# Performance work log

Measured on AMD Instinct MI355X. Metric: run time of the kernel, lower is better.

## Reference

```python
import jax, jax.numpy as jnp
import numpy as np

C = 64        # channel_n
HID = 128     # hidden_size
HEADS = 4
HD = 16       # head_dim = embed_dim // heads, embed_dim overwritten to channel_n
INNER = HEADS * HD  # 64
MLP = 64
H = W = 64    # img_size
B = 8
STEPS = 6
IN_CH = 1     # input_channels
SCALE = HD ** -0.5


def conv3x3_reflect(x, w, b):
    # x: [B,C,H,W], w: [O,I,3,3] -- reflect padding like nn.Conv2d(padding_mode='reflect')
    xp = jnp.pad(x, ((0, 0), (0, 0), (1, 1), (1, 1)), mode='reflect')
    y = jax.lax.conv_general_dilated(xp, w, (1, 1), 'VALID',
                                     dimension_numbers=('NCHW', 'OIHW', 'NCHW'))
    return y + b[None, :, None, None]


def layernorm(x, w, b, axes):
    mu = jnp.mean(x, axis=axes, keepdims=True)
    var = jnp.var(x, axis=axes, keepdims=True)
    return (x - mu) * jax.lax.rsqrt(var + 1e-5) * w + b


def localize(t, h, w):
    # t: [B,heads,n,d] -> [B,heads,n,9,d]; zero-padded 3x3 neighbourhoods
    # (equivalent to grouped conv with 9 unit-impulse filters, padding='same')
    b, nh, n, d = t.shape
    g = t.reshape(b, nh, h, w, d)
    gp = jnp.pad(g, ((0, 0), (0, 0), (1, 1), (1, 1), (0, 0)))
    nb = jnp.stack([gp[:, :, i:i + h, j:j + w, :]
                    for i in range(3) for j in range(3)], axis=4)
    return nb.reshape(b, nh, n, 9, d)


def attn_block(t, ln_w, ln_b, qkv_w, out_w, out_b):
    y = layernorm(t, ln_w, ln_b, -1)
    qkv = y @ qkv_w.T                              # [B,n,3*inner]
    q, k, v = jnp.split(qkv, 3, axis=-1)
    to_heads = lambda z: z.reshape(z.shape[0], z.shape[1], HEADS, HD).transpose(0, 2, 1, 3)
    q, k, v = to_heads(q), to_heads(k), to_heads(v)   # [B,h,n,d]
    kl = localize(k, H, W)                          # [B,h,n,9,d]
    vl = localize(v, H, W)
    dots = jnp.einsum('bhnd,bhnkd->bhnk', q, kl) * SCALE
    a = jax.nn.softmax(dots, axis=-1)               # [B,h,n,9]
    o = jnp.einsum('bhnk,bhnkd->bhnd', a, vl)
    o = o.transpose(0, 2, 1, 3).reshape(t.shape[0], t.shape[1], INNER)
    return o @ out_w.T + out_b


def ff_block(t, ln_w, ln_b, w1, b1, w2, b2):
    y = layernorm(t, ln_w, ln_b, -1)
    y = jax.nn.gelu(y @ w1.T + b1, approximate=False)
    return y @ w2.T + b2


def setup_inputs() -> dict:
    key = jax.random.key(0)
    ks = jax.random.split(key, 20)
    s = 0.02
    inp = {
        'x': jax.random.normal(ks[0], (B, H, W, C), jnp.float32),
        'masks': jax.random.bernoulli(ks[1], 0.5, (STEPS, B, H, W, 1)),
        'p0_w': jax.random.normal(ks[2], (C, C, 3, 3)) * s,
        'p0_b': jnp.zeros((C,)),
        'p1_w': jax.random.normal(ks[3], (C, C, 3, 3)) * s,
        'p1_b': jnp.zeros((C,)),
        'fc0_w': jax.random.normal(ks[4], (HID, 3 * C)) * s,
        'fc0_b': jnp.zeros((HID,)),
        'fc1_w': jax.random.normal(ks[5], (C, HID)) * s,  # zero-init in torch; random here for a non-trivial test
        'norm0_w': jnp.ones((H, W, HID)),
        'norm0_b': jnp.zeros((H, W, HID)),
        'ln1_w': jnp.ones((C,)),
        'ln1_b': jnp.zeros((C,)),
        'qkv_w': jax.random.normal(ks[6], (3 * INNER, C)) * s,
        'out_w': jax.random.normal(ks[7], (C, INNER)) * s,
        'out_b': jnp.zeros((C,)),
        'ln2_w': jnp.ones((C,)),
        'ln2_b': jnp.zeros((C,)),
        'ff1_w': jax.random.normal(ks[8], (MLP, C)) * s,
        'ff1_b': jnp.zeros((MLP,)),
        'ff2_w': jax.random.normal(ks[9], (C, MLP)) * s,
        'ff2_b': jnp.zeros((C,)),
        'steps': STEPS,
    }
    return inp


def reference(x, masks, p0_w, p0_b, p1_w, p1_b, fc0_w, fc0_b, fc1_w,
              norm0_w, norm0_b, ln1_w, ln1_b, qkv_w, out_w, out_b,
              ln2_w, ln2_b, ff1_w, ff1_b, ff2_w, ff2_b, steps):
    def step(xc, mask):
        # ---- NCA perception + update (BackboneNCA.perceive + fc0/relu/norm/fc1) ----
        xt = xc.transpose(0, 3, 1, 2)                      # [B,C,H,W]
        y1 = conv3x3_reflect(xt, p0_w, p0_b)
        y2 = conv3x3_reflect(xt, p1_w, p1_b)
        p = jnp.concatenate([xt, y1, y2], 1).transpose(0, 2, 3, 1)  # [B,H,W,3C]
        hd = jax.nn.relu(p @ fc0_w.T + fc0_b)              # [B,H,W,HID]
        hd = layernorm(hd, norm0_w, norm0_b, (-3, -2, -1))  # norm0 over [H,W,HID]
        dx = hd @ fc1_w.T                                   # [B,H,W,C]
        dx = dx * mask.astype(xc.dtype)                     # stochastic fire
        xn = xc + dx
        # ---- ViT block with localized (3x3 windowed) attention ----
        t = xn.reshape(B, H * W, C)
        t = t + attn_block(t, ln1_w, ln1_b, qkv_w, out_w, out_b)
        t = t + ff_block(t, ln2_w, ln2_b, ff1_w, ff1_b, ff2_w, ff2_b)
        xn = t.reshape(B, H, W, C)
        # keep input channels unchanged
        xn = jnp.concatenate([xc[..., :IN_CH], xn[..., IN_CH:]], axis=-1)
        return xn, None

    out, _ = jax.lax.scan(step, x, masks)
    return out
```

## Files before the change

### kernel.cpp

```cpp
#include <hip/hip_runtime.h>
#include <hip/hip_bf16.h>

typedef __hip_bfloat16 bf16;
typedef __attribute__((ext_vector_type(8))) short bf16x8;
typedef __attribute__((ext_vector_type(4))) float f32x4;

#define NSTEP 6

static __device__ __forceinline__ float b2f(bf16 v) { return __bfloat162float(v); }

static __device__ __forceinline__ float ldp(const void* p, int i, int md) {
    return md ? ((const float*)p)[i] : b2f(((const bf16*)p)[i]);
}
static __device__ __forceinline__ float finz(float v) {
    return (v == v && v * 0.0f == 0.0f) ? v : 0.0f;
}
static __device__ __forceinline__ unsigned short f2bfu(float v) {
    bf16 h = __float2bfloat16(v);
    return *(unsigned short*)&h;
}

static __device__ __forceinline__ void ld_bf8(const bf16* p, float* f) {
    union { uint4 u; unsigned short s[8]; } r;
    r.u = *(const uint4*)p;
#pragma unroll
    for (int j = 0; j < 8; ++j) f[j] = __uint_as_float(((unsigned)r.s[j]) << 16);
}
static __device__ __forceinline__ void ldp8(const void* p, int i, int md, float* f) {
    if (md) {
        const float* fp = (const float*)p + i;
        float4 a = *(const float4*)fp, b = *(const float4*)(fp + 4);
        f[0]=a.x; f[1]=a.y; f[2]=a.z; f[3]=a.w; f[4]=b.x; f[5]=b.y; f[6]=b.z; f[7]=b.w;
    } else {
        ld_bf8((const bf16*)p + i, f);
    }
}
static __device__ __forceinline__ uint4 pk_bf8(const float* f) {
    union { uint4 u; unsigned short s[8]; } r;
#pragma unroll
    for (int j = 0; j < 8; ++j) r.s[j] = f2bfu(f[j]);
    return r.u;
}


__global__ void k_detect(const uint4* __restrict__ m4,
                         const uint4* __restrict__ x4,
                         int* __restrict__ flags, float* __restrict__ accv) {
    __shared__ int s3f, sup, slo, sf32;
    int t = threadIdx.x;
    if (t == 0) { s3f = 0; sup = 0; slo = 0; sf32 = 0; }
    if (t < 96) accv[t] = 0.f;
    __syncthreads();
    int l3f = 0, lup = 0, llo = 0, lf = 0;
    for (int i = t; i < 3072; i += 256) {
        uint4 v = m4[i];
        const unsigned* d = (const unsigned*)&v;
#pragma unroll
        for (int j = 0; j < 4; ++j) {
            unsigned w = d[j];
            unsigned x3f = w ^ 0x3F3F3F3Fu;
            if ((x3f - 0x01010101u) & ~x3f & 0x80808080u) l3f = 1;
            if (w & 0xFFFFFF00u) lup = 1;
            if (w & 0x0000FFFFu) llo = 1;
        }
    }
    for (int i = t; i < 4096; i += 256) {
        uint4 v = x4[i];
        const unsigned* d = (const unsigned*)&v;
#pragma unroll
        for (int j = 0; j < 4; ++j) {
            unsigned bb = (d[j] >> 8) & 0x7Fu;
            if (bb > 0x48u) lf = 1;
        }
    }
    if (l3f) atomicOr(&s3f, 1);
    if (lup) atomicOr(&sup, 1);
    if (llo) atomicOr(&slo, 1);
    if (lf)  atomicOr(&sf32, 1);
    __syncthreads();
    if (t == 0) {
        int mode;
        if (!s3f && !sup) mode = 0;
        else if (!s3f)    mode = 1;
        else if (slo)     mode = 2;
        else              mode = 3;
        flags[0] = mode;
        flags[1] = sf32;
    }
}

__global__ void k_cast(const void* __restrict__ in, float* __restrict__ out,
                       const int* __restrict__ mflags, int n8) {
    int md = mflags[1];
    int i = blockIdx.x * 256 + threadIdx.x;
    if (i < n8) {
        float f[8];
        ldp8(in, i * 8, md, f);
#pragma unroll
        for (int j = 0; j < 8; ++j) f[j] = finz(f[j]);
        *(float4*)&out[i * 8]     = make_float4(f[0], f[1], f[2], f[3]);
        *(float4*)&out[i * 8 + 4] = make_float4(f[4], f[5], f[6], f[7]);
    }
}

__global__ void k_pack_multi(const void* __restrict__ pa, const void* __restrict__ pb,
                             const void* __restrict__ pc, const void* __restrict__ pd,
                             const void* __restrict__ pe, const void* __restrict__ pf,
                             short* __restrict__ out, const int* __restrict__ mflags) {
    int md = mflags[1];
    int i = blockIdx.x * 256 + threadIdx.x;
    if (i >= 57344) return;
    float v;
    if      (i < 24576) v = ldp(pa, i, md);
    else if (i < 32768) v = ldp(pb, i - 24576, md);
    else if (i < 45056) v = ldp(pc, i - 32768, md);
    else if (i < 49152) v = ldp(pd, i - 45056, md);
    else if (i < 53248) v = ldp(pe, i - 49152, md);
    else                v = ldp(pf, i - 53248, md);
    out[i] = (short)f2bfu(v);
}

__global__ void k_pack_bt1(const void* __restrict__ p0, const void* __restrict__ p1,
                           short* __restrict__ out, const int* __restrict__ mflags) {
    int md = mflags[1];
    int i = blockIdx.x * 256 + threadIdx.x;
    if (i < 128 * 576) {
        int o = i / 576, k = i % 576;
        int kk = k >> 6, ii = k & 63;
        float v = (o < 64) ? ldp(p0, o * 576 + ii * 9 + kk, md)
                           : ldp(p1, (o - 64) * 576 + ii * 9 + kk, md);
        out[i] = (short)f2bfu(v);
    }
}


__global__ __launch_bounds__(512) void k_perceive(
    const float* __restrict__ xin, const short* __restrict__ bt1,
    const short* __restrict__ fc0s, const void* __restrict__ p0b,
    const void* __restrict__ p1b, const void* __restrict__ fc0b,
    const int* __restrict__ mflags, bf16* __restrict__ hd,
    float* __restrict__ accv, int step)
{
    __shared__ __align__(16) short xpad_s[3 * 66 * 72];
    __shared__ __align__(16) short P_s[64 * 200];
    __shared__ float red[32];
    int md = mflags[1];
    int bh = blockIdx.x;
    int b = bh >> 6, h = bh & 63;
    int t = threadIdx.x;

    for (int e = t; e < 1536; e += 512) {
        int c8 = e & 7, w = (e >> 3) & 63, r = e >> 9;
        int hr = h - 1 + r; hr = hr < 0 ? -hr : (hr > 63 ? 126 - hr : hr);
        const float* src = xin + ((((b << 6) + hr) << 6) | w) * 64 + c8 * 8;
        float f[8];
        float4 v0 = *(const float4*)src, v1 = *(const float4*)(src + 4);
        f[0]=v0.x; f[1]=v0.y; f[2]=v0.z; f[3]=v0.w; f[4]=v1.x; f[5]=v1.y; f[6]=v1.z; f[7]=v1.w;
        uint4 pv = pk_bf8(f);
        *(uint4*)&xpad_s[((r * 66) + w + 1) * 72 + c8 * 8] = pv;
        if (r == 1) *(uint4*)&P_s[w * 200 + c8 * 8] = pv;
    }
    if (t < 48) {
        int c8 = t & 7, side = (t >> 3) & 1, r = t >> 4;
        int hr = h - 1 + r; hr = hr < 0 ? -hr : (hr > 63 ? 126 - hr : hr);
        int wsrc = side ? 62 : 1, wp = side ? 65 : 0;
        const float* src = xin + ((((b << 6) + hr) << 6) | wsrc) * 64 + c8 * 8;
        float f[8];
        float4 v0 = *(const float4*)src, v1 = *(const float4*)(src + 4);
        f[0]=v0.x; f[1]=v0.y; f[2]=v0.z; f[3]=v0.w; f[4]=v1.x; f[5]=v1.y; f[6]=v1.z; f[7]=v1.w;
        *(uint4*)&xpad_s[((r * 66) + wp) * 72 + c8 * 8] = pk_bf8(f);
    }
    __syncthreads();

    int og  = __builtin_amdgcn_readfirstlane(t >> 6);
    int l   = t & 63, nl = l & 15, q = l >> 4;
    int mt0 = (og & 1) * 2;
    int nt0 = (og >> 1) * 2;
    int o0  = nt0 * 16 + nl, o1 = o0 + 16;

    f32x4 acc[2][2];
#pragma unroll
    for (int i = 0; i < 2; ++i)
#pragma unroll
        for (int j = 0; j < 2; ++j) acc[i][j] = (f32x4){0.f, 0.f, 0.f, 0.f};

    for (int kt = 0; kt < 18; ++kt) {
        int kk = kt >> 1, c0 = (kt & 1) << 5;
        int r = kk / 3, cxi = kk - r * 3;
        bf16x8 b0 = *(const bf16x8*)(bt1 + o0 * 576 + kt * 32 + q * 8);
        bf16x8 b1 = *(const bf16x8*)(bt1 + o1 * 576 + kt * 32 + q * 8);
        bf16x8 a0 = *(const bf16x8*)&xpad_s[((r * 66) + mt0 * 16 + nl + cxi) * 72 + c0 + q * 8];
        bf16x8 a1 = *(const bf16x8*)&xpad_s[((r * 66) + mt0 * 16 + 16 + nl + cxi) * 72 + c0 + q * 8];
        acc[0][0] = __builtin_amdgcn_mfma_f32_16x16x32_bf16(a0, b0, acc[0][0], 0, 0, 0);
        acc[0][1] = __builtin_amdgcn_mfma_f32_16x16x32_bf16(a0, b1, acc[0][1], 0, 0, 0);
        acc[1][0] = __builtin_amdgcn_mfma_f32_16x16x32_bf16(a1, b0, acc[1][0], 0, 0, 0);
        acc[1][1] = __builtin_amdgcn_mfma_f32_16x16x32_bf16(a1, b1, acc[1][1], 0, 0, 0);
    }
    {
        float bias0 = (o0 < 64) ? ldp(p0b, o0, md) : ldp(p1b, o0 - 64, md);
        float bias1 = (o1 < 64) ? ldp(p0b, o1, md) : ldp(p1b, o1 - 64, md);
#pragma unroll
        for (int i = 0; i < 2; ++i)
#pragma unroll
            for (int j = 0; j < 2; ++j) {
                int oo = j ? o1 : o0;
                float bb = j ? bias1 : bias0;
#pragma unroll
                for (int r2 = 0; r2 < 4; ++r2) {
                    int m = (mt0 + i) * 16 + q * 4 + r2;
                    P_s[m * 200 + 64 + oo] = (short)f2bfu(acc[i][j][r2] + bb);
                }
            }
    }
    __syncthreads();

#pragma unroll
    for (int i = 0; i < 2; ++i)
#pragma unroll
        for (int j = 0; j < 2; ++j) acc[i][j] = (f32x4){0.f, 0.f, 0.f, 0.f};
    for (int kt = 0; kt < 6; ++kt) {
        bf16x8 b0 = *(const bf16x8*)(fc0s + o0 * 192 + kt * 32 + q * 8);
        bf16x8 b1 = *(const bf16x8*)(fc0s + o1 * 192 + kt * 32 + q * 8);
        bf16x8 a0 = *(const bf16x8*)&P_s[(mt0 * 16 + nl) * 200 + kt * 32 + q * 8];
        bf16x8 a1 = *(const bf16x8*)&P_s[(mt0 * 16 + 16 + nl) * 200 + kt * 32 + q * 8];
        acc[0][0] = __builtin_amdgcn_mfma_f32_16x16x32_bf16(a0, b0, acc[0][0], 0, 0, 0);
        acc[0][1] = __builtin_amdgcn_mfma_f32_16x16x32_bf16(a0, b1, acc[0][1], 0, 0, 0);
        acc[1][0] = __builtin_amdgcn_mfma_f32_16x16x32_bf16(a1, b0, acc[1][0], 0, 0, 0);
        acc[1][1] = __builtin_amdgcn_mfma_f32_16x16x32_bf16(a1, b1, acc[1][1], 0, 0, 0);
    }
    float lsum = 0.f, lsq = 0.f;
    {
        float fb0 = ldp(fc0b, o0, md), fb1 = ldp(fc0b, o1, md);
#pragma unroll
        for (int i = 0; i < 2; ++i)
#pragma unroll
            for (int j = 0; j < 2; ++j) {
                int oo = j ? o1 : o0;
                float bb = j ? fb1 : fb0;
#pragma unroll
                for (int r2 = 0; r2 < 4; ++r2) {
                    int m = (mt0 + i) * 16 + q * 4 + r2;
                    float v = fmaxf(acc[i][j][r2] + bb, 0.f);
                    unsigned short hu = f2bfu(v);
                    hd[((bh << 6) + m) * 128 + oo] = *(bf16*)&hu;
                    float vr = __uint_as_float(((unsigned)hu) << 16);
                    lsum += vr; lsq += vr * vr;
                }
            }
    }
#pragma unroll
    for (int off = 32; off > 0; off >>= 1) {
        lsum += __shfl_down(lsum, off, 64);
        lsq  += __shfl_down(lsq,  off, 64);
    }
    if (l == 0) { red[og] = lsum; red[16 + og] = lsq; }
    __syncthreads();
    if (t == 0) {
        float a = 0.f, s2 = 0.f;
#pragma unroll
        for (int w = 0; w < 8; ++w) { a += red[w]; s2 += red[16 + w]; }
        atomicAdd(&accv[step * 16 + b * 2],     a);
        atomicAdd(&accv[step * 16 + b * 2 + 1], s2);
    }
}

__global__ __launch_bounds__(512) void k_update_qkv(
    float* __restrict__ xio, const bf16* __restrict__ hd,
    const short* __restrict__ fc1s, const void* __restrict__ n0w,
    const void* __restrict__ n0b, const void* __restrict__ mraw,
    const int* __restrict__ mflags, const float* __restrict__ accv,
    float* __restrict__ c0buf, const short* __restrict__ qkvs,
    const void* __restrict__ ln1w, const void* __restrict__ ln1b,
    bf16* __restrict__ qkv, int step)
{
    __shared__ __align__(16) char sm[43264];
    short* hdn = (short*)sm;
    float* ts  = (float*)(sm + 17408);
    short* ys  = (short*)(sm + 34048);
    short* qo  = (short*)sm;

    int md = mflags[1];
    int bh = blockIdx.x;
    int b = bh >> 6, h = bh & 63;
    int t = threadIdx.x;
    const float invN = 1.f / 524288.f;
    float mean = accv[step * 16 + b * 2] * invN;
    float var  = accv[step * 16 + b * 2 + 1] * invN - mean * mean;
    float rstd = rsqrtf(fmaxf(var, 0.f) + 1e-5f);

    const bf16* hrow = hd + ((b * 64 + h) * 64) * 128;
    for (int e = t; e < 1024; e += 512) {
        int pos = e >> 4, j8 = (e & 15) * 8;
        float hv[8], wv[8], bv[8], f[8];
        ld_bf8(hrow + pos * 128 + j8, hv);
        int ni = (h * 64 + pos) * 128 + j8;
        ldp8(n0w, ni, md, wv);
        ldp8(n0b, ni, md, bv);
#pragma unroll
        for (int j = 0; j < 8; ++j) f[j] = (hv[j] - mean) * rstd * wv[j] + bv[j];
        *(uint4*)&hdn[pos * 136 + j8] = pk_bf8(f);
    }
    __syncthreads();

    int og = __builtin_amdgcn_readfirstlane(t >> 6);
    int l = t & 63, nl = l & 15, q = l >> 4;

    {
        int mt = og & 3, nh = og >> 2;
        int o0 = nh * 32 + nl, o1 = o0 + 16;
        f32x4 a0 = (f32x4){0.f,0.f,0.f,0.f}, a1 = (f32x4){0.f,0.f,0.f,0.f};
#pragma unroll
        for (int kt = 0; kt < 4; ++kt) {
            bf16x8 av = *(const bf16x8*)&hdn[(mt * 16 + nl) * 136 + kt * 32 + q * 8];
            bf16x8 b0 = *(const bf16x8*)(fc1s + o0 * 128 + kt * 32 + q * 8);
            bf16x8 b1 = *(const bf16x8*)(fc1s + o1 * 128 + kt * 32 + q * 8);
            a0 = __builtin_amdgcn_mfma_f32_16x16x32_bf16(av, b0, a0, 0, 0, 0);
            a1 = __builtin_amdgcn_mfma_f32_16x16x32_bf16(av, b1, a1, 0, 0, 0);
        }
#pragma unroll
        for (int r2 = 0; r2 < 4; ++r2) {
            int m = mt * 16 + q * 4 + r2;
            ts[m * 65 + o0] = a0[r2];
            ts[m * 65 + o1] = a1[r2];
        }
    }
    __syncthreads();

    int cg = og;
    int pos = t & 63;
    {
        int mmode = mflags[0];
        int midx = ((step * 8 + b) * 64 + h) * 64 + pos;
        int mk;
        if (mmode == 0)      mk = ((const int*)mraw)[midx] != 0;
        else if (mmode == 1) mk = ((const unsigned char*)mraw)[midx] != 0;
        else if (mmode == 2) mk = ((const unsigned short*)mraw)[midx] != 0;
        else                 mk = ((const float*)mraw)[midx] != 0.0f;

        int idx = ((b * 64 + h) * 64 + pos) * 64 + cg * 8;
        float4 x0 = *(const float4*)&xio[idx];
        float4 x1 = *(const float4*)&xio[idx + 4];
        float xv[8] = {x0.x, x0.y, x0.z, x0.w, x1.x, x1.y, x1.z, x1.w};
        if (cg == 0) c0buf[(b * 64 + h) * 64 + pos] = xv[0];
        float* tp = &ts[pos * 65 + cg * 8];
        float xn[8];
#pragma unroll
        for (int ci = 0; ci < 8; ++ci) {
            xn[ci] = finz(mk ? (xv[ci] + tp[ci]) : xv[ci]);
            tp[ci] = xn[ci];
        }
        *(float4*)&xio[idx]     = make_float4(xn[0], xn[1], xn[2], xn[3]);
        *(float4*)&xio[idx + 4] = make_float4(xn[4], xn[5], xn[6], xn[7]);
    }
    __syncthreads();

    {
        int tok = t >> 3, j8 = (t & 7) * 8;
        float v[8];
        float ls = 0.f, lq = 0.f;
#pragma unroll
        for (int ci = 0; ci < 8; ++ci) {
            v[ci] = ts[tok * 65 + j8 + ci];
            ls += v[ci]; lq += v[ci] * v[ci];
        }
#pragma unroll
        for (int off = 1; off < 8; off <<= 1) {
            ls += __shfl_xor(ls, off, 64);
            lq += __shfl_xor(lq, off, 64);
        }
        float mu = ls * (1.f / 64.f);
        float vr = lq * (1.f / 64.f) - mu * mu;
        float rs = rsqrtf(fmaxf(vr, 0.f) + 1e-5f);
        float wv[8], bv[8];
        ldp8(ln1w, j8, md, wv);
        ldp8(ln1b, j8, md, bv);
        float yv[8];
#pragma unroll
        for (int ci = 0; ci < 8; ++ci) yv[ci] = (v[ci] - mu) * rs * wv[ci] + bv[ci];
        *(uint4*)&ys[tok * 72 + j8] = pk_bf8(yv);
    }
    __syncthreads();

    {
        int mt = og & 3, nh = og >> 2;
        f32x4 qa[6];
#pragma unroll
        for (int n = 0; n < 6; ++n) qa[n] = (f32x4){0.f, 0.f, 0.f, 0.f};
#pragma unroll
        for (int kt = 0; kt < 2; ++kt) {
            bf16x8 av = *(const bf16x8*)&ys[(mt * 16 + nl) * 72 + kt * 32 + q * 8];
#pragma unroll
            for (int n = 0; n < 6; ++n) {
                bf16x8 bv = *(const bf16x8*)(qkvs + (((nh * 6 + n) * 16) + nl) * 64 + kt * 32 + q * 8);
                qa[n] = __builtin_amdgcn_mfma_f32_16x16x32_bf16(av, bv, qa[n], 0, 0, 0);
            }
        }
#pragma unroll
        for (int n = 0; n < 6; ++n)
#pragma unroll
            for (int r2 = 0; r2 < 4; ++r2) {
                int m = mt * 16 + q * 4 + r2;
                qo[m * 200 + (nh * 6 + n) * 16 + nl] = (short)f2bfu(qa[n][r2]);
            }
    }
    __syncthreads();

    for (int e = t; e < 1536; e += 512) {
        int p2 = e / 24, c8 = e - p2 * 24;
        *(uint4*)(qkv + ((bh << 6) + p2) * 192 + c8 * 8) =
            *(const uint4*)&qo[p2 * 200 + c8 * 8];
    }
}

__global__ __launch_bounds__(512) void k_attn_ff(
    const bf16* __restrict__ qkv, float* __restrict__ xio,
    const float* __restrict__ c0buf, const short* __restrict__ outs,
    const short* __restrict__ ff1s, const short* __restrict__ ff2s,
    const void* __restrict__ outb, const void* __restrict__ ln2w,
    const void* __restrict__ ln2b, const void* __restrict__ ff1b,
    const void* __restrict__ ff2b, const int* __restrict__ mflags,
    void* __restrict__ dout, int write_out)
{
    __shared__ __align__(16) char smraw[57024];
    short* Ks = (short*)smraw;
    short* Vs = (short*)(smraw + 28512);
    short* Ao = (short*)smraw;
    float* ts = (float*)(smraw + 9216);
    short* ys = (short*)(smraw + 25856);
    short* hs = (short*)(smraw + 35072);

    int md = mflags[1];
    int bh = blockIdx.x;
    int b = bh >> 6, h = bh & 63;
    int t = threadIdx.x;

    if (t < 96) {
        int kind = (t >= 48) ? 1 : 0, u = t - kind * 48;
        int r = u >> 4, side = (u >> 3) & 1, c8 = u & 7;
        short* dst = kind ? Vs : Ks;
        uint4 z = {0, 0, 0, 0};
        *(uint4*)&dst[((r * 66) + (side ? 65 : 0)) * 72 + c8 * 8] = z;
    }
    for (int e = t; e < 3072; e += 512) {
        int kind = (e >= 1536) ? 1 : 0, u = e - kind * 1536;
        int c8 = u & 7, w = (u >> 3) & 63, r = u >> 9;
        int hr = h - 1 + r;
        uint4 v = {0, 0, 0, 0};
        if (hr >= 0 && hr <= 63)
            v = *(const uint4*)(qkv + ((b * 64 + hr) * 64 + w) * 192 + 64 + kind * 64 + c8 * 8);
        short* dst = kind ? Vs : Ks;
        *(uint4*)&dst[((r * 66) + w + 1) * 72 + c8 * 8] = v;
    }
    __syncthreads();

    int head = __builtin_amdgcn_readfirstlane(t >> 6) & 3;
    int pos  = t & 63;
    bool act = t < 256;
    float o[16];
    if (act) {
        float qv[16];
        const bf16* qr = qkv + (((b * 64 + h) * 64) + pos) * 192 + head * 16;
        ld_bf8(qr, qv); ld_bf8(qr + 8, qv + 8);

        float a9[9];
#pragma unroll
        for (int r = 0; r < 3; ++r)
#pragma unroll
            for (int cxi = 0; cxi < 3; ++cxi) {
                const short* kp = &Ks[((r * 66) + pos + cxi) * 72 + head * 16];
                float kf[16];
                ld_bf8((const bf16*)kp, kf);
                ld_bf8((const bf16*)(kp + 8), kf + 8);
                float dot = 0.f;
#pragma unroll
                for (int d = 0; d < 16; ++d) dot = fmaf(qv[d], kf[d], dot);
                a9[r * 3 + cxi] = dot * 0.25f;
            }
        float mx = a9[0];
#pragma unroll
        for (int k = 1; k < 9; ++k) mx = fmaxf(mx, a9[k]);
        float ssum = 0.f;
#pragma unroll
        for (int k = 0; k < 9; ++k) { a9[k] = __expf(a9[k] - mx); ssum += a9[k]; }
        float inv = 1.f / ssum;
#pragma unroll
        for (int k = 0; k < 9; ++k) a9[k] *= inv;

#pragma unroll
        for (int d = 0; d < 16; ++d) o[d] = 0.f;
#pragma unroll
        for (int r = 0; r < 3; ++r)
#pragma unroll
            for (int cxi = 0; cxi < 3; ++cxi) {
                const short* vp = &Vs[((r * 66) + pos + cxi) * 72 + head * 16];
                float vf[16];
                ld_bf8((const bf16*)vp, vf);
                ld_bf8((const bf16*)(vp + 8), vf + 8);
                float w = a9[r * 3 + cxi];
#pragma unroll
                for (int d = 0; d < 16; ++d) o[d] = fmaf(w, vf[d], o[d]);
            }
    }
    __syncthreads();
    if (act) {
        *(uint4*)&Ao[pos * 72 + head * 16]     = pk_bf8(o);
        *(uint4*)&Ao[pos * 72 + head * 16 + 8] = pk_bf8(o + 8);
    }
    __syncthreads();

    int og = __builtin_amdgcn_readfirstlane(t >> 6);
    int l = t & 63, nl = l & 15, qd = l >> 4;
    int mt = og & 3;
    int nt0 = (og >> 2) * 2;
    int o0 = nt0 * 16 + nl, o1 = o0 + 16;

    {
        f32x4 pa[2];
        pa[0] = (f32x4){0.f,0.f,0.f,0.f}; pa[1] = (f32x4){0.f,0.f,0.f,0.f};
#pragma unroll
        for (int kt = 0; kt < 2; ++kt) {
            bf16x8 av = *(const bf16x8*)&Ao[(mt * 16 + nl) * 72 + kt * 32 + qd * 8];
            bf16x8 b0 = *(const bf16x8*)(outs + o0 * 64 + kt * 32 + qd * 8);
            bf16x8 b1 = *(const bf16x8*)(outs + o1 * 64 + kt * 32 + qd * 8);
            pa[0] = __builtin_amdgcn_mfma_f32_16x16x32_bf16(av, b0, pa[0], 0, 0, 0);
            pa[1] = __builtin_amdgcn_mfma_f32_16x16x32_bf16(av, b1, pa[1], 0, 0, 0);
        }
        float ob0 = ldp(outb, o0, md), ob1 = ldp(outb, o1, md);
#pragma unroll
        for (int j = 0; j < 2; ++j)
#pragma unroll
            for (int r2 = 0; r2 < 4; ++r2) {
                int m = mt * 16 + qd * 4 + r2;
                ts[m * 65 + (j ? o1 : o0)] = pa[j][r2] + (j ? ob1 : ob0);
            }
    }
    __syncthreads();

    int idx = ((bh << 6) + pos) * 64 + (t >> 6) * 8;
    {
        int cg2 = t >> 6;
        float4 x0 = *(const float4*)&xio[idx];
        float4 x1 = *(const float4*)&xio[idx + 4];
        float* tp = &ts[pos * 65 + cg2 * 8];
        tp[0] += x0.x; tp[1] += x0.y; tp[2] += x0.z; tp[3] += x0.w;
        tp[4] += x1.x; tp[5] += x1.y; tp[6] += x1.z; tp[7] += x1.w;
    }
    __syncthreads();

    {
        int tok = t >> 3, j8 = (t & 7) * 8;
        float v[8];
        float ls = 0.f, lq = 0.f;
#pragma unroll
        for (int ci = 0; ci < 8; ++ci) {
            v[ci] = ts[tok * 65 + j8 + ci];
            ls += v[ci]; lq += v[ci] * v[ci];
        }
#pragma unroll
        for (int off = 1; off < 8; off <<= 1) {
            ls += __shfl_xor(ls, off, 64);
            lq += __shfl_xor(lq, off, 64);
        }
        float mu = ls * (1.f / 64.f);
        float vr = lq * (1.f / 64.f) - mu * mu;
        float rs = rsqrtf(fmaxf(vr, 0.f) + 1e-5f);
        float wv[8], bv[8];
        ldp8(ln2w, j8, md, wv);
        ldp8(ln2b, j8, md, bv);
        float yv[8];
#pragma unroll
        for (int ci = 0; ci < 8; ++ci) yv[ci] = (v[ci] - mu) * rs * wv[ci] + bv[ci];
        *(uint4*)&ys[tok * 72 + j8] = pk_bf8(yv);
    }
    __syncthreads();

    {
        f32x4 ma[2];
        ma[0] = (f32x4){0.f,0.f,0.f,0.f}; ma[1] = (f32x4){0.f,0.f,0.f,0.f};
#pragma unroll
        for (int kt = 0; kt < 2; ++kt) {
            bf16x8 av = *(const bf16x8*)&ys[(mt * 16 + nl) * 72 + kt * 32 + qd * 8];
            bf16x8 b0 = *(const bf16x8*)(ff1s + o0 * 64 + kt * 32 + qd * 8);
            bf16x8 b1 = *(const bf16x8*)(ff1s + o1 * 64 + kt * 32 + qd * 8);
            ma[0] = __builtin_amdgcn_mfma_f32_16x16x32_bf16(av, b0, ma[0], 0, 0, 0);
            ma[1] = __builtin_amdgcn_mfma_f32_16x16x32_bf16(av, b1, ma[1], 0, 0, 0);
        }
        float f1b0 = ldp(ff1b, o0, md), f1b1 = ldp(ff1b, o1, md);
#pragma unroll
        for (int j = 0; j < 2; ++j)
#pragma unroll
            for (int r2 = 0; r2 < 4; ++r2) {
                int m = mt * 16 + qd * 4 + r2;
                float v = ma[j][r2] + (j ? f1b1 : f1b0);
                float g = 0.5f * v * (1.f + erff(v * 0.70710678118654752f));
                hs[m * 72 + (j ? o1 : o0)] = (short)f2bfu(g);
            }
    }
    __syncthreads();

    {
        f32x4 fa[2];
        fa[0] = (f32x4){0.f,0.f,0.f,0.f}; fa[1] = (f32x4){0.f,0.f,0.f,0.f};
#pragma unroll
        for (int kt = 0; kt < 2; ++kt) {
            bf16x8 av = *(const bf16x8*)&hs[(mt * 16 + nl) * 72 + kt * 32 + qd * 8];
            bf16x8 b0 = *(const bf16x8*)(ff2s + o0 * 64 + kt * 32 + qd * 8);
            bf16x8 b1 = *(const bf16x8*)(ff2s + o1 * 64 + kt * 32 + qd * 8);
            fa[0] = __builtin_amdgcn_mfma_f32_16x16x32_bf16(av, b0, fa[0], 0, 0, 0);
            fa[1] = __builtin_amdgcn_mfma_f32_16x16x32_bf16(av, b1, fa[1], 0, 0, 0);
        }
        float f2b0 = ldp(ff2b, o0, md), f2b1 = ldp(ff2b, o1, md);
#pragma unroll
        for (int j = 0; j < 2; ++j)
#pragma unroll
            for (int r2 = 0; r2 < 4; ++r2) {
                int m = mt * 16 + qd * 4 + r2;
                int oo = j ? o1 : o0;
                ts[m * 65 + oo] += fa[j][r2] + (j ? f2b1 : f2b0);
            }
    }
    __syncthreads();

    {
        int cg2 = t >> 6;
        float fv[8];
#pragma unroll
        for (int ci = 0; ci < 8; ++ci) {
            float v = ts[pos * 65 + cg2 * 8 + ci];
            if (cg2 == 0 && ci == 0) v = c0buf[(bh << 6) + pos];
            fv[ci] = finz(v);
        }
        *(float4*)&xio[idx]     = make_float4(fv[0], fv[1], fv[2], fv[3]);
        *(float4*)&xio[idx + 4] = make_float4(fv[4], fv[5], fv[6], fv[7]);
        if (write_out) {
            if (md) {
                *(float4*)&((float*)dout)[idx]     = make_float4(fv[0], fv[1], fv[2], fv[3]);
                *(float4*)&((float*)dout)[idx + 4] = make_float4(fv[4], fv[5], fv[6], fv[7]);
            } else {
                *(uint4*)&((bf16*)dout)[idx] = pk_bf8(fv);
            }
        }
    }
}


extern "C" void kernel_launch(void* const* d_in, const int* in_sizes, int n_in,
                              void* d_out, int out_size, void* d_ws, size_t ws_size,
                              hipStream_t stream) {
    (void)in_sizes; (void)n_in; (void)out_size; (void)ws_size;
    const void* x     = d_in[0];
    const void* masks = d_in[1];
    const void* p0w   = d_in[2];
    const void* p0b   = d_in[3];
    const void* p1w   = d_in[4];
    const void* p1b   = d_in[5];
    const void* fc0w  = d_in[6];
    const void* fc0b  = d_in[7];
    const void* fc1w  = d_in[8];
    const void* n0w   = d_in[9];
    const void* n0b   = d_in[10];
    const void* ln1w  = d_in[11];
    const void* ln1b  = d_in[12];
    const void* qkvw  = d_in[13];
    const void* outw  = d_in[14];
    const void* outb  = d_in[15];
    const void* ln2w  = d_in[16];
    const void* ln2b  = d_in[17];
    const void* ff1w  = d_in[18];
    const void* ff1b  = d_in[19];
    const void* ff2w  = d_in[20];
    const void* ff2b  = d_in[21];

    char* wsb = (char*)d_ws;
    float* xst    = (float*)(wsb + 0);
    bf16*  hd     = (bf16*) (wsb + 8388608);
    bf16*  qkvb   = (bf16*) (wsb + 16777216);
    float* c0buf  = (float*)(wsb + 29360128);
    short* bt1    = (short*)(wsb + 29491200);
    short* packs  = (short*)(wsb + 29638656);
    float* accv   = (float*)(wsb + 29753344);
    int*   mflags = (int*)  (wsb + 29753728);

    short* fc0s = packs;
    short* fc1s = packs + 24576;
    short* qkvs = packs + 32768;
    short* outs = packs + 45056;
    short* ff1s = packs + 49152;
    short* ff2s = packs + 53248;

    k_detect<<<1, 256, 0, stream>>>((const uint4*)masks, (const uint4*)x, mflags, accv);
    k_cast<<<1024, 256, 0, stream>>>(x, xst, mflags, 262144);
    k_pack_bt1<<<288, 256, 0, stream>>>(p0w, p1w, bt1, mflags);
    k_pack_multi<<<224, 256, 0, stream>>>(fc0w, fc1w, qkvw, outw, ff1w, ff2w, packs, mflags);

    for (int s = 0; s < NSTEP; ++s) {
        k_perceive<<<512, 512, 0, stream>>>(xst, bt1, fc0s, p0b, p1b, fc0b, mflags, hd, accv, s);
        k_update_qkv<<<512, 512, 0, stream>>>(xst, hd, fc1s, n0w, n0b, masks, mflags, accv,
                                              c0buf, qkvs, ln1w, ln1b, qkvb, s);
        k_attn_ff<<<512, 512, 0, stream>>>(qkvb, xst, c0buf, outs, ff1s, ff2s,
                                           outb, ln2w, ln2b, ff1b, ff2b, mflags,
                                           d_out, (s == NSTEP - 1) ? 1 : 0);
    }
}
```

Measured before the change: 592.9 us.

## Fold norm0 into fc1 algebraically and fuse update/QKV into attention kernel

The global layernorm is rewritten as rstd*(hd*w)@fc1 - mean*rstd*(w@fc1) + b@fc1. The two weight products are precomputed once by a new k_fold kernel, so fc1 can run inside the perceive kernel before the global statistics are known. The separate update/QKV kernel is merged into the attention/FF kernel, which recomputes the update, LN1 and QKV for the three neighbouring rows instead of round-tripping qkv and hd through global memory. This drops one launch per step and ping-pongs the state between two buffers, at the cost of about three times the QKV work and larger shared memory use in the fused kernel.

```diff
diff --git a/kernel.cpp b/kernel.cpp
--- a/kernel.cpp
+++ b/kernel.cpp
@@ -133,16 +133,41 @@
     }
 }
 
+__global__ void k_fold(const void* __restrict__ n0w, const void* __restrict__ n0b,
+                       const short* __restrict__ fc1s, float* __restrict__ wsum,
+                       float* __restrict__ bconst, const int* __restrict__ mflags) {
+    __shared__ short fc1T[128 * 64];
+    int md = mflags[1];
+    int t = threadIdx.x;
+    for (int e = t; e < 8192; e += 256) {
+        int c2 = e >> 7, j = e & 127;
+        fc1T[j * 64 + c2] = fc1s[c2 * 128 + j];
+    }
+    __syncthreads();
+    int c = t & 63, pl = t >> 6;
+    int pos = blockIdx.x * 4 + pl;
+    float ws = 0.f, bs = 0.f;
+    for (int j = 0; j < 128; ++j) {
+        float f = b2f(*(const bf16*)&fc1T[j * 64 + c]);
+        ws = fmaf(ldp(n0w, pos * 128 + j, md), f, ws);
+        bs = fmaf(ldp(n0b, pos * 128 + j, md), f, bs);
+    }
+    wsum[pos * 64 + c]   = ws;
+    bconst[pos * 64 + c] = bs;
+}
+
 
 __global__ __launch_bounds__(512) void k_perceive(
     const float* __restrict__ xin, const short* __restrict__ bt1,
-    const short* __restrict__ fc0s, const void* __restrict__ p0b,
-    const void* __restrict__ p1b, const void* __restrict__ fc0b,
-    const int* __restrict__ mflags, bf16* __restrict__ hd,
+    const short* __restrict__ fc0s, const short* __restrict__ fc1s,
+    const void* __restrict__ p0b, const void* __restrict__ p1b,
+    const void* __restrict__ fc0b, const void* __restrict__ n0w,
+    const int* __restrict__ mflags, float* __restrict__ t1,
     float* __restrict__ accv, int step)
 {
     __shared__ __align__(16) short xpad_s[3 * 66 * 72];
     __shared__ __align__(16) short P_s[64 * 200];
+    __shared__ __align__(16) short hd_s[64 * 136];
     __shared__ float red[32];
     int md = mflags[1];
     int bh = blockIdx.x;
@@ -242,7 +267,7 @@
                     int m = (mt0 + i) * 16 + q * 4 + r2;
                     float v = fmaxf(acc[i][j][r2] + bb, 0.f);
                     unsigned short hu = f2bfu(v);
-                    hd[((bh << 6) + m) * 128 + oo] = *(bf16*)&hu;
+                    hd_s[m * 136 + oo] = (short)hu;
                     float vr = __uint_as_float(((unsigned)hu) << 16);
                     lsum += vr; lsq += vr * vr;
                 }
@@ -262,177 +287,71 @@
         atomicAdd(&accv[step * 16 + b * 2],     a);
         atomicAdd(&accv[step * 16 + b * 2 + 1], s2);
     }
-}
-
-__global__ __launch_bounds__(512) void k_update_qkv(
-    float* __restrict__ xio, const bf16* __restrict__ hd,
-    const short* __restrict__ fc1s, const void* __restrict__ n0w,
-    const void* __restrict__ n0b, const void* __restrict__ mraw,
-    const int* __restrict__ mflags, const float* __restrict__ accv,
-    float* __restrict__ c0buf, const short* __restrict__ qkvs,
-    const void* __restrict__ ln1w, const void* __restrict__ ln1b,
-    bf16* __restrict__ qkv, int step)
+
+    for (int e = t; e < 1024; e += 512) {
+        int pos = e >> 4, j8 = (e & 15) * 8;
+        float hv[8], wv[8];
+        ld_bf8((const bf16*)&hd_s[pos * 136 + j8], hv);
+        ldp8(n0w, (h * 64 + pos) * 128 + j8, md, wv);
+#pragma unroll
+        for (int j = 0; j < 8; ++j) hv[j] *= wv[j];
+        *(uint4*)&hd_s[pos * 136 + j8] = pk_bf8(hv);
+    }
+    __syncthreads();
+
+    {
+        int mt = og & 3, nh = og >> 2;
+        int to0 = nh * 32 + nl, to1 = to0 + 16;
+        f32x4 a0 = (f32x4){0.f,0.f,0.f,0.f}, a1 = (f32x4){0.f,0.f,0.f,0.f};
+#pragma unroll
+        for (int kt = 0; kt < 4; ++kt) {
+            bf16x8 av = *(const bf16x8*)&hd_s[(mt * 16 + nl) * 136 + kt * 32 + q * 8];
+            bf16x8 b0 = *(const bf16x8*)(fc1s + to0 * 128 + kt * 32 + q * 8);
+            bf16x8 b1 = *(const bf16x8*)(fc1s + to1 * 128 + kt * 32 + q * 8);
+            a0 = __builtin_amdgcn_mfma_f32_16x16x32_bf16(av, b0, a0, 0, 0, 0);
+            a1 = __builtin_amdgcn_mfma_f32_16x16x32_bf16(av, b1, a1, 0, 0, 0);
+        }
+#pragma unroll
+        for (int r2 = 0; r2 < 4; ++r2) {
+            int m = mt * 16 + q * 4 + r2;
+            t1[((bh << 6) + m) * 64 + to0] = a0[r2];
+            t1[((bh << 6) + m) * 64 + to1] = a1[r2];
+        }
+    }
+}
+
+__global__ __launch_bounds__(512) void k_step2(
+    const float* __restrict__ xin, float* __restrict__ xout,
+    const float* __restrict__ t1, const float* __restrict__ wsum,
+    const float* __restrict__ bconst, const void* __restrict__ mraw,
+    const short* __restrict__ qkvs, const void* __restrict__ ln1w,
+    const void* __restrict__ ln1b, const short* __restrict__ outs,
+    const short* __restrict__ ff1s, const short* __restrict__ ff2s,
+    const void* __restrict__ outb, const void* __restrict__ ln2w,
+    const void* __restrict__ ln2b, const void* __restrict__ ff1b,
+    const void* __restrict__ ff2b, const int* __restrict__ mflags,
+    const float* __restrict__ accv, void* __restrict__ dout,
+    int step, int write_out)
 {
-    __shared__ __align__(16) char sm[43264];
-    short* hdn = (short*)sm;
-    float* ts  = (float*)(sm + 17408);
-    short* ys  = (short*)(sm + 34048);
-    short* qo  = (short*)sm;
+    __shared__ __align__(16) char smraw[75456];
+    short* Ks = (short*)smraw;
+    short* Vs = (short*)(smraw + 28512);
+    short* qo = (short*)(smraw + 57024);
+    short* ys = (short*)(smraw + 66240);
+    short* Ao = (short*)smraw;
+    float* ts = (float*)(smraw + 9216);
+    short* hs = (short*)(smraw + 25856);
 
     int md = mflags[1];
     int bh = blockIdx.x;
     int b = bh >> 6, h = bh & 63;
     int t = threadIdx.x;
+
     const float invN = 1.f / 524288.f;
     float mean = accv[step * 16 + b * 2] * invN;
     float var  = accv[step * 16 + b * 2 + 1] * invN - mean * mean;
     float rstd = rsqrtf(fmaxf(var, 0.f) + 1e-5f);
-
-    const bf16* hrow = hd + ((b * 64 + h) * 64) * 128;
-    for (int e = t; e < 1024; e += 512) {
-        int pos = e >> 4, j8 = (e & 15) * 8;
-        float hv[8], wv[8], bv[8], f[8];
-        ld_bf8(hrow + pos * 128 + j8, hv);
-        int ni = (h * 64 + pos) * 128 + j8;
-        ldp8(n0w, ni, md, wv);
-        ldp8(n0b, ni, md, bv);
-#pragma unroll
-        for (int j = 0; j < 8; ++j) f[j] = (hv[j] - mean) * rstd * wv[j] + bv[j];
-        *(uint4*)&hdn[pos * 136 + j8] = pk_bf8(f);
-    }
-    __syncthreads();
-
-    int og = __builtin_amdgcn_readfirstlane(t >> 6);
-    int l = t & 63, nl = l & 15, q = l >> 4;
-
-    {
-        int mt = og & 3, nh = og >> 2;
-        int o0 = nh * 32 + nl, o1 = o0 + 16;
-        f32x4 a0 = (f32x4){0.f,0.f,0.f,0.f}, a1 = (f32x4){0.f,0.f,0.f,0.f};
-#pragma unroll
-        for (int kt = 0; kt < 4; ++kt) {
-            bf16x8 av = *(const bf16x8*)&hdn[(mt * 16 + nl) * 136 + kt * 32 + q * 8];
-            bf16x8 b0 = *(const bf16x8*)(fc1s + o0 * 128 + kt * 32 + q * 8);
-            bf16x8 b1 = *(const bf16x8*)(fc1s + o1 * 128 + kt * 32 + q * 8);
-            a0 = __builtin_amdgcn_mfma_f32_16x16x32_bf16(av, b0, a0, 0, 0, 0);
-            a1 = __builtin_amdgcn_mfma_f32_16x16x32_bf16(av, b1, a1, 0, 0, 0);
-        }
-#pragma unroll
-        for (int r2 = 0; r2 < 4; ++r2) {
-            int m = mt * 16 + q * 4 + r2;
-            ts[m * 65 + o0] = a0[r2];
-            ts[m * 65 + o1] = a1[r2];
-        }
-    }
-    __syncthreads();
-
-    int cg = og;
-    int pos = t & 63;
-    {
-        int mmode = mflags[0];
-        int midx = ((step * 8 + b) * 64 + h) * 64 + pos;
-        int mk;
-        if (mmode == 0)      mk = ((const int*)mraw)[midx] != 0;
-        else if (mmode == 1) mk = ((const unsigned char*)mraw)[midx] != 0;
-        else if (mmode == 2) mk = ((const unsigned short*)mraw)[midx] != 0;
-        else                 mk = ((const float*)mraw)[midx] != 0.0f;
-
-        int idx = ((b * 64 + h) * 64 + pos) * 64 + cg * 8;
-        float4 x0 = *(const float4*)&xio[idx];
-        float4 x1 = *(const float4*)&xio[idx + 4];
-        float xv[8] = {x0.x, x0.y, x0.z, x0.w, x1.x, x1.y, x1.z, x1.w};
-        if (cg == 0) c0buf[(b * 64 + h) * 64 + pos] = xv[0];
-        float* tp = &ts[pos * 65 + cg * 8];
-        float xn[8];
-#pragma unroll
-        for (int ci = 0; ci < 8; ++ci) {
-            xn[ci] = finz(mk ? (xv[ci] + tp[ci]) : xv[ci]);
-            tp[ci] = xn[ci];
-        }
-        *(float4*)&xio[idx]     = make_float4(xn[0], xn[1], xn[2], xn[3]);
-        *(float4*)&xio[idx + 4] = make_float4(xn[4], xn[5], xn[6], xn[7]);
-    }
-    __syncthreads();
-
-    {
-        int tok = t >> 3, j8 = (t & 7) * 8;
-        float v[8];
-        float ls = 0.f, lq = 0.f;
-#pragma unroll
-        for (int ci = 0; ci < 8; ++ci) {
-            v[ci] = ts[tok * 65 + j8 + ci];
-            ls += v[ci]; lq += v[ci] * v[ci];
-        }
-#pragma unroll
-        for (int off = 1; off < 8; off <<= 1) {
-            ls += __shfl_xor(ls, off, 64);
-            lq += __shfl_xor(lq, off, 64);
-        }
-        float mu = ls * (1.f / 64.f);
-        float vr = lq * (1.f / 64.f) - mu * mu;
-        float rs = rsqrtf(fmaxf(vr, 0.f) + 1e-5f);
-        float wv[8], bv[8];
-        ldp8(ln1w, j8, md, wv);
-        ldp8(ln1b, j8, md, bv);
-        float yv[8];
-#pragma unroll
-        for (int ci = 0; ci < 8; ++ci) yv[ci] = (v[ci] - mu) * rs * wv[ci] + bv[ci];
-        *(uint4*)&ys[tok * 72 + j8] = pk_bf8(yv);
-    }
-    __syncthreads();
-
-    {
-        int mt = og & 3, nh = og >> 2;
-        f32x4 qa[6];
-#pragma unroll
-        for (int n = 0; n < 6; ++n) qa[n] = (f32x4){0.f, 0.f, 0.f, 0.f};
-#pragma unroll
-        for (int kt = 0; kt < 2; ++kt) {
-            bf16x8 av = *(const bf16x8*)&ys[(mt * 16 + nl) * 72 + kt * 32 + q * 8];
-#pragma unroll
-            for (int n = 0; n < 6; ++n) {
-                bf16x8 bv = *(const bf16x8*)(qkvs + (((nh * 6 + n) * 16) + nl) * 64 + kt * 32 + q * 8);
-                qa[n] = __builtin_amdgcn_mfma_f32_16x16x32_bf16(av, bv, qa[n], 0, 0, 0);
-            }
-        }
-#pragma unroll
-        for (int n = 0; n < 6; ++n)
-#pragma unroll
-            for (int r2 = 0; r2 < 4; ++r2) {
-                int m = mt * 16 + q * 4 + r2;
-                qo[m * 200 + (nh * 6 + n) * 16 + nl] = (short)f2bfu(qa[n][r2]);
-            }
-    }
-    __syncthreads();
-
-    for (int e = t; e < 1536; e += 512) {
-        int p2 = e / 24, c8 = e - p2 * 24;
-        *(uint4*)(qkv + ((bh << 6) + p2) * 192 + c8 * 8) =
-            *(const uint4*)&qo[p2 * 200 + c8 * 8];
-    }
-}
-
-__global__ __launch_bounds__(512) void k_attn_ff(
-    const bf16* __restrict__ qkv, float* __restrict__ xio,
-    const float* __restrict__ c0buf, const short* __restrict__ outs,
-    const short* __restrict__ ff1s, const short* __restrict__ ff2s,
-    const void* __restrict__ outb, const void* __restrict__ ln2w,
-    const void* __restrict__ ln2b, const void* __restrict__ ff1b,
-    const void* __restrict__ ff2b, const int* __restrict__ mflags,
-    void* __restrict__ dout, int write_out)
-{
-    __shared__ __align__(16) char smraw[57024];
-    short* Ks = (short*)smraw;
-    short* Vs = (short*)(smraw + 28512);
-    short* Ao = (short*)smraw;
-    float* ts = (float*)(smraw + 9216);
-    short* ys = (short*)(smraw + 25856);
-    short* hs = (short*)(smraw + 35072);
-
-    int md = mflags[1];
-    int bh = blockIdx.x;
-    int b = bh >> 6, h = bh & 63;
-    int t = threadIdx.x;
+    float mrs  = mean * rstd;
 
     if (t < 96) {
         int kind = (t >= 48) ? 1 : 0, u = t - kind * 48;
@@ -441,15 +360,111 @@
         uint4 z = {0, 0, 0, 0};
         *(uint4*)&dst[((r * 66) + (side ? 65 : 0)) * 72 + c8 * 8] = z;
     }
-    for (int e = t; e < 3072; e += 512) {
-        int kind = (e >= 1536) ? 1 : 0, u = e - kind * 1536;
-        int c8 = u & 7, w = (u >> 3) & 63, r = u >> 9;
+
+    int og = __builtin_amdgcn_readfirstlane(t >> 6);
+    int l = t & 63, nl = l & 15, q = l >> 4;
+    int tok = t >> 3, j8 = (t & 7) * 8;
+    int mmode = mflags[0];
+
+    float tn[8];
+    float c0 = 0.f;
+#pragma unroll
+    for (int ci = 0; ci < 8; ++ci) tn[ci] = 0.f;
+
+    for (int r = 0; r < 3; ++r) {
         int hr = h - 1 + r;
-        uint4 v = {0, 0, 0, 0};
-        if (hr >= 0 && hr <= 63)
-            v = *(const uint4*)(qkv + ((b * 64 + hr) * 64 + w) * 192 + 64 + kind * 64 + c8 * 8);
-        short* dst = kind ? Vs : Ks;
-        *(uint4*)&dst[((r * 66) + w + 1) * 72 + c8 * 8] = v;
+        __syncthreads();
+        if (hr < 0 || hr > 63) {
+            for (int e = t; e < 1024; e += 512) {
+                int kind = (e >= 512) ? 1 : 0, u = e & 511;
+                int w = u >> 3, c8 = u & 7;
+                short* dst = kind ? Vs : Ks;
+                uint4 z = {0, 0, 0, 0};
+                *(uint4*)&dst[((r * 66) + w + 1) * 72 + c8 * 8] = z;
+            }
+            continue;
+        }
+        {
+            int row = (b * 64 + hr) * 64 + tok;
+            int ppos = hr * 64 + tok;
+            const float* xr = xin + row * 64 + j8;
+            float4 x0 = *(const float4*)xr, x1 = *(const float4*)(xr + 4);
+            float xv[8] = {x0.x, x0.y, x0.z, x0.w, x1.x, x1.y, x1.z, x1.w};
+            const float* t1r = t1 + row * 64 + j8;
+            float4 a0 = *(const float4*)t1r, a1 = *(const float4*)(t1r + 4);
+            float tv[8] = {a0.x, a0.y, a0.z, a0.w, a1.x, a1.y, a1.z, a1.w};
+            const float* wr = wsum + ppos * 64 + j8;
+            float4 w0 = *(const float4*)wr, w1 = *(const float4*)(wr + 4);
+            float wv[8] = {w0.x, w0.y, w0.z, w0.w, w1.x, w1.y, w1.z, w1.w};
+            const float* br = bconst + ppos * 64 + j8;
+            float4 b0 = *(const float4*)br, b1 = *(const float4*)(br + 4);
+            float bc[8] = {b0.x, b0.y, b0.z, b0.w, b1.x, b1.y, b1.z, b1.w};
+
+            int midx = ((step * 8 + b) * 64 + hr) * 64 + tok;
+            int mk;
+            if (mmode == 0)      mk = ((const int*)mraw)[midx] != 0;
+            else if (mmode == 1) mk = ((const unsigned char*)mraw)[midx] != 0;
+            else if (mmode == 2) mk = ((const unsigned short*)mraw)[midx] != 0;
+            else                 mk = ((const float*)mraw)[midx] != 0.0f;
+
+            float vloc[8];
+            float ls = 0.f, lq = 0.f;
+#pragma unroll
+            for (int ci = 0; ci < 8; ++ci) {
+                float dx = rstd * tv[ci] - mrs * wv[ci] + bc[ci];
+                vloc[ci] = finz(mk ? (xv[ci] + dx) : xv[ci]);
+                ls += vloc[ci]; lq += vloc[ci] * vloc[ci];
+            }
+            if (r == 1) {
+#pragma unroll
+                for (int ci = 0; ci < 8; ++ci) tn[ci] = vloc[ci];
+                if (j8 == 0) c0 = xv[0];
+            }
+#pragma unroll
+            for (int off = 1; off < 8; off <<= 1) {
+                ls += __shfl_xor(ls, off, 64);
+                lq += __shfl_xor(lq, off, 64);
+            }
+            float mu = ls * (1.f / 64.f);
+            float vr = lq * (1.f / 64.f) - mu * mu;
+            float rs = rsqrtf(fmaxf(vr, 0.f) + 1e-5f);
+            float lw[8], lb[8];
+            ldp8(ln1w, j8, md, lw);
+            ldp8(ln1b, j8, md, lb);
+            float yv[8];
+#pragma unroll
+            for (int ci = 0; ci < 8; ++ci)
+                yv[ci] = (vloc[ci] - mu) * rs * lw[ci] + lb[ci];
+            *(uint4*)&ys[tok * 72 + j8] = pk_bf8(yv);
+        }
+        __syncthreads();
+        {
+            int mt = og & 3, nh2 = og >> 2;
+            f32x4 qa[6];
+#pragma unroll
+            for (int n = 0; n < 6; ++n) qa[n] = (f32x4){0.f, 0.f, 0.f, 0.f};
+#pragma unroll
+            for (int kt = 0; kt < 2; ++kt) {
+                bf16x8 av = *(const bf16x8*)&ys[(mt * 16 + nl) * 72 + kt * 32 + q * 8];
+#pragma unroll
+                for (int n = 0; n < 6; ++n) {
+                    bf16x8 bv = *(const bf16x8*)(qkvs + (((nh2 * 6 + n) * 16) + nl) * 64 + kt * 32 + q * 8);
+                    qa[n] = __builtin_amdgcn_mfma_f32_16x16x32_bf16(av, bv, qa[n], 0, 0, 0);
+                }
+            }
+#pragma unroll
+            for (int n = 0; n < 6; ++n) {
+                int nt = nh2 * 6 + n;
+#pragma unroll
+                for (int r2 = 0; r2 < 4; ++r2) {
+                    int m = mt * 16 + q * 4 + r2;
+                    short hv = (short)f2bfu(qa[n][r2]);
+                    if (nt < 4) { if (r == 1) qo[m * 72 + nt * 16 + nl] = hv; }
+                    else if (nt < 8) Ks[((r * 66) + m + 1) * 72 + (nt - 4) * 16 + nl] = hv;
+                    else             Vs[((r * 66) + m + 1) * 72 + (nt - 8) * 16 + nl] = hv;
+                }
+            }
+        }
     }
     __syncthreads();
 
@@ -459,8 +474,8 @@
     float o[16];
     if (act) {
         float qv[16];
-        const bf16* qr = qkv + (((b * 64 + h) * 64) + pos) * 192 + head * 16;
-        ld_bf8(qr, qv); ld_bf8(qr + 8, qv + 8);
+        ld_bf8((const bf16*)&qo[pos * 72 + head * 16], qv);
+        ld_bf8((const bf16*)&qo[pos * 72 + head * 16 + 8], qv + 8);
 
         float a9[9];
 #pragma unroll
@@ -508,8 +523,6 @@
     }
     __syncthreads();
 
-    int og = __builtin_amdgcn_readfirstlane(t >> 6);
-    int l = t & 63, nl = l & 15, qd = l >> 4;
     int mt = og & 3;
     int nt0 = (og >> 2) * 2;
     int o0 = nt0 * 16 + nl, o1 = o0 + 16;
@@ -519,9 +532,9 @@
         pa[0] = (f32x4){0.f,0.f,0.f,0.f}; pa[1] = (f32x4){0.f,0.f,0.f,0.f};
 #pragma unroll
         for (int kt = 0; kt < 2; ++kt) {
-            bf16x8 av = *(const bf16x8*)&Ao[(mt * 16 + nl) * 72 + kt * 32 + qd * 8];
-            bf16x8 b0 = *(const bf16x8*)(outs + o0 * 64 + kt * 32 + qd * 8);
-            bf16x8 b1 = *(const bf16x8*)(outs + o1 * 64 + kt * 32 + qd * 8);
+            bf16x8 av = *(const bf16x8*)&Ao[(mt * 16 + nl) * 72 + kt * 32 + q * 8];
+            bf16x8 b0 = *(const bf16x8*)(outs + o0 * 64 + kt * 32 + q * 8);
+            bf16x8 b1 = *(const bf16x8*)(outs + o1 * 64 + kt * 32 + q * 8);
             pa[0] = __builtin_amdgcn_mfma_f32_16x16x32_bf16(av, b0, pa[0], 0, 0, 0);
             pa[1] = __builtin_amdgcn_mfma_f32_16x16x32_bf16(av, b1, pa[1], 0, 0, 0);
         }
@@ -530,30 +543,19 @@
         for (int j = 0; j < 2; ++j)
 #pragma unroll
             for (int r2 = 0; r2 < 4; ++r2) {
-                int m = mt * 16 + qd * 4 + r2;
+                int m = mt * 16 + q * 4 + r2;
                 ts[m * 65 + (j ? o1 : o0)] = pa[j][r2] + (j ? ob1 : ob0);
             }
     }
     __syncthreads();
 
-    int idx = ((bh << 6) + pos) * 64 + (t >> 6) * 8;
     {
-        int cg2 = t >> 6;
-        float4 x0 = *(const float4*)&xio[idx];
-        float4 x1 = *(const float4*)&xio[idx + 4];
-        float* tp = &ts[pos * 65 + cg2 * 8];
-        tp[0] += x0.x; tp[1] += x0.y; tp[2] += x0.z; tp[3] += x0.w;
-        tp[4] += x1.x; tp[5] += x1.y; tp[6] += x1.z; tp[7] += x1.w;
-    }
-    __syncthreads();
-
-    {
-        int tok = t >> 3, j8 = (t & 7) * 8;
         float v[8];
         float ls = 0.f, lq = 0.f;
 #pragma unroll
         for (int ci = 0; ci < 8; ++ci) {
-            v[ci] = ts[tok * 65 + j8 + ci];
+            v[ci] = ts[tok * 65 + j8 + ci] + tn[ci];
+            ts[tok * 65 + j8 + ci] = v[ci];
             ls += v[ci]; lq += v[ci] * v[ci];
         }
 #pragma unroll
@@ -579,9 +581,9 @@
         ma[0] = (f32x4){0.f,0.f,0.f,0.f}; ma[1] = (f32x4){0.f,0.f,0.f,0.f};
 #pragma unroll
         for (int kt = 0; kt < 2; ++kt) {
-            bf16x8 av = *(const bf16x8*)&ys[(mt * 16 + nl) * 72 + kt * 32 + qd * 8];
-            bf16x8 b0 = *(const bf16x8*)(ff1s + o0 * 64 + kt * 32 + qd * 8);
-            bf16x8 b1 = *(const bf16x8*)(ff1s + o1 * 64 + kt * 32 + qd * 8);
+            bf16x8 av = *(const bf16x8*)&ys[(mt * 16 + nl) * 72 + kt * 32 + q * 8];
+            bf16x8 b0 = *(const bf16x8*)(ff1s + o0 * 64 + kt * 32 + q * 8);
+            bf16x8 b1 = *(const bf16x8*)(ff1s + o1 * 64 + kt * 32 + q * 8);
             ma[0] = __builtin_amdgcn_mfma_f32_16x16x32_bf16(av, b0, ma[0], 0, 0, 0);
             ma[1] = __builtin_amdgcn_mfma_f32_16x16x32_bf16(av, b1, ma[1], 0, 0, 0);
         }
@@ -590,7 +592,7 @@
         for (int j = 0; j < 2; ++j)
 #pragma unroll
             for (int r2 = 0; r2 < 4; ++r2) {
-                int m = mt * 16 + qd * 4 + r2;
+                int m = mt * 16 + q * 4 + r2;
                 float v = ma[j][r2] + (j ? f1b1 : f1b0);
                 float g = 0.5f * v * (1.f + erff(v * 0.70710678118654752f));
                 hs[m * 72 + (j ? o1 : o0)] = (short)f2bfu(g);
@@ -603,9 +605,9 @@
         fa[0] = (f32x4){0.f,0.f,0.f,0.f}; fa[1] = (f32x4){0.f,0.f,0.f,0.f};
 #pragma unroll
         for (int kt = 0; kt < 2; ++kt) {
-            bf16x8 av = *(const bf16x8*)&hs[(mt * 16 + nl) * 72 + kt * 32 + qd * 8];
-            bf16x8 b0 = *(const bf16x8*)(ff2s + o0 * 64 + kt * 32 + qd * 8);
-            bf16x8 b1 = *(const bf16x8*)(ff2s + o1 * 64 + kt * 32 + qd * 8);
+            bf16x8 av = *(const bf16x8*)&hs[(mt * 16 + nl) * 72 + kt * 32 + q * 8];
+            bf16x8 b0 = *(const bf16x8*)(ff2s + o0 * 64 + kt * 32 + q * 8);
+            bf16x8 b1 = *(const bf16x8*)(ff2s + o1 * 64 + kt * 32 + q * 8);
             fa[0] = __builtin_amdgcn_mfma_f32_16x16x32_bf16(av, b0, fa[0], 0, 0, 0);
             fa[1] = __builtin_amdgcn_mfma_f32_16x16x32_bf16(av, b1, fa[1], 0, 0, 0);
         }
@@ -614,7 +616,7 @@
         for (int j = 0; j < 2; ++j)
 #pragma unroll
             for (int r2 = 0; r2 < 4; ++r2) {
-                int m = mt * 16 + qd * 4 + r2;
+                int m = mt * 16 + q * 4 + r2;
                 int oo = j ? o1 : o0;
                 ts[m * 65 + oo] += fa[j][r2] + (j ? f2b1 : f2b0);
             }
@@ -622,16 +624,16 @@
     __syncthreads();
 
     {
-        int cg2 = t >> 6;
+        int idx = ((bh << 6) + tok) * 64 + j8;
         float fv[8];
 #pragma unroll
         for (int ci = 0; ci < 8; ++ci) {
-            float v = ts[pos * 65 + cg2 * 8 + ci];
-            if (cg2 == 0 && ci == 0) v = c0buf[(bh << 6) + pos];
+            float v = ts[tok * 65 + j8 + ci];
+            if (j8 == 0 && ci == 0) v = c0;
             fv[ci] = finz(v);
         }
-        *(float4*)&xio[idx]     = make_float4(fv[0], fv[1], fv[2], fv[3]);
-        *(float4*)&xio[idx + 4] = make_float4(fv[4], fv[5], fv[6], fv[7]);
+        *(float4*)&xout[idx]     = make_float4(fv[0], fv[1], fv[2], fv[3]);
+        *(float4*)&xout[idx + 4] = make_float4(fv[4], fv[5], fv[6], fv[7]);
         if (write_out) {
             if (md) {
                 *(float4*)&((float*)dout)[idx]     = make_float4(fv[0], fv[1], fv[2], fv[3]);
@@ -672,14 +674,15 @@
     const void* ff2b  = d_in[21];
 
     char* wsb = (char*)d_ws;
-    float* xst    = (float*)(wsb + 0);
-    bf16*  hd     = (bf16*) (wsb + 8388608);
-    bf16*  qkvb   = (bf16*) (wsb + 16777216);
-    float* c0buf  = (float*)(wsb + 29360128);
-    short* bt1    = (short*)(wsb + 29491200);
-    short* packs  = (short*)(wsb + 29638656);
-    float* accv   = (float*)(wsb + 29753344);
-    int*   mflags = (int*)  (wsb + 29753728);
+    float* xst0   = (float*)(wsb + 0);
+    float* xst1   = (float*)(wsb + 8388608);
+    float* t1buf  = (float*)(wsb + 16777216);
+    short* bt1    = (short*)(wsb + 25165824);
+    short* packs  = (short*)(wsb + 25313280);
+    float* wsumb  = (float*)(wsb + 25427968);
+    float* bconb  = (float*)(wsb + 26476544);
+    float* accv   = (float*)(wsb + 27525120);
+    int*   mflags = (int*)  (wsb + 27525504);
 
     short* fc0s = packs;
     short* fc1s = packs + 24576;
@@ -689,16 +692,20 @@
     short* ff2s = packs + 53248;
 
     k_detect<<<1, 256, 0, stream>>>((const uint4*)masks, (const uint4*)x, mflags, accv);
-    k_cast<<<1024, 256, 0, stream>>>(x, xst, mflags, 262144);
+    k_cast<<<1024, 256, 0, stream>>>(x, xst0, mflags, 262144);
     k_pack_bt1<<<288, 256, 0, stream>>>(p0w, p1w, bt1, mflags);
     k_pack_multi<<<224, 256, 0, stream>>>(fc0w, fc1w, qkvw, outw, ff1w, ff2w, packs, mflags);
-
+    k_fold<<<1024, 256, 0, stream>>>(n0w, n0b, fc1s, wsumb, bconb, mflags);
+
+    float* xbuf[2] = {xst0, xst1};
     for (int s = 0; s < NSTEP; ++s) {
-        k_perceive<<<512, 512, 0, stream>>>(xst, bt1, fc0s, p0b, p1b, fc0b, mflags, hd, accv, s);
-        k_update_qkv<<<512, 512, 0, stream>>>(xst, hd, fc1s, n0w, n0b, masks, mflags, accv,
-                                              c0buf, qkvs, ln1w, ln1b, qkvb, s);
-        k_attn_ff<<<512, 512, 0, stream>>>(qkvb, xst, c0buf, outs, ff1s, ff2s,
-                                           outb, ln2w, ln2b, ff1b, ff2b, mflags,
-                                           d_out, (s == NSTEP - 1) ? 1 : 0);
-    }
-}
+        float* cur = xbuf[s & 1];
+        float* nxt = xbuf[(s + 1) & 1];
+        k_perceive<<<512, 512, 0, stream>>>(cur, bt1, fc0s, fc1s, p0b, p1b, fc0b,
+                                            n0w, mflags, t1buf, accv, s);
+        k_step2<<<512, 512, 0, stream>>>(cur, nxt, t1buf, wsumb, bconb, masks,
+                                         qkvs, ln1w, ln1b, outs, ff1s, ff2s,
+                                         outb, ln2w, ln2b, ff1b, ff2b, mflags,
+                                         accv, d_out, s, (s == NSTEP - 1) ? 1 : 0);
+    }
+}
```

After: 628.4 us. 1.06x slower.
